# Optimization experiments

Hardware: AMD Instinct MI355X
Metric: run time of the kernel (lower is better)

## Reference

```python
import jax, jax.numpy as jnp
import numpy as np

NEG_SLOPE = 0.2
EPS = 1e-16


def gat_layer(x, src, dst, W, att_src, att_dst, bias, heads, concat):
    N = x.shape[0]
    C = W.shape[1] // heads
    h = (x @ W).reshape(N, heads, C)                      # [N,H,C]
    a_src = (h * att_src).sum(-1)                         # [N,H]
    a_dst = (h * att_dst).sum(-1)                         # [N,H]
    e = jax.nn.leaky_relu(a_src[src] + a_dst[dst], NEG_SLOPE)  # [E,H]
    # numerically-stable softmax over incoming edges of each dst node
    e_max = jax.ops.segment_max(e, dst, num_segments=N)   # [N,H]
    e_max = jnp.where(jnp.isfinite(e_max), e_max, 0.0)
    ex = jnp.exp(e - e_max[dst])                          # [E,H]
    denom = jax.ops.segment_sum(ex, dst, num_segments=N) + EPS
    alpha = ex / denom[dst]                               # [E,H]
    msg = alpha[:, :, None] * h[src]                      # [E,H,C]
    out = jax.ops.segment_sum(msg, dst, num_segments=N)   # [N,H,C]
    if concat:
        return out.reshape(N, heads * C) + bias
    return out.mean(axis=1) + bias


def setup_inputs() -> dict:
    key = jax.random.key(0)
    ks = jax.random.split(key, 12)
    N, E = 50000, 800000
    IN, HID, OUT, H = 128, 8, 40, 8
    x = jax.random.normal(ks[0], (N, IN), dtype=jnp.float32)
    edge_index = jax.random.randint(ks[1], (2, E), 0, N, dtype=jnp.int64)
    s1 = 1.0 / np.sqrt(IN)
    s2 = 1.0 / np.sqrt(HID * H)
    W1 = jax.random.normal(ks[2], (IN, H * HID), dtype=jnp.float32) * s1
    att_src1 = jax.random.normal(ks[3], (H, HID), dtype=jnp.float32) * 0.1
    att_dst1 = jax.random.normal(ks[4], (H, HID), dtype=jnp.float32) * 0.1
    bias1 = jnp.zeros((H * HID,), dtype=jnp.float32)
    W2 = jax.random.normal(ks[5], (H * HID, OUT), dtype=jnp.float32) * s2
    att_src2 = jax.random.normal(ks[6], (1, OUT), dtype=jnp.float32) * 0.1
    att_dst2 = jax.random.normal(ks[7], (1, OUT), dtype=jnp.float32) * 0.1
    bias2 = jnp.zeros((OUT,), dtype=jnp.float32)
    return {"x": x, "edge_index": edge_index,
            "W1": W1, "att_src1": att_src1, "att_dst1": att_dst1, "bias1": bias1,
            "W2": W2, "att_src2": att_src2, "att_dst2": att_dst2, "bias2": bias2}


def reference(x, edge_index, W1, att_src1, att_dst1, bias1, W2, att_src2, att_dst2, bias2):
    src, dst = edge_index[0], edge_index[1]
    # eval mode: dropout is identity
    h = gat_layer(x, src, dst, W1, att_src1, att_dst1, bias1, heads=8, concat=True)
    h = jax.nn.elu(h)
    out = gat_layer(h, src, dst, W2, att_src2, att_dst2, bias2, heads=1, concat=False)
    return out
```

## Files before the change

kernel.cpp:

```cpp
#include <hip/hip_runtime.h>
#include <math.h>

#define EPS 1e-16f
#define SLOT 64
__device__ __forceinline__ float lrelu(float v) { return v > 0.0f ? v : 0.2f * v; }

__device__ __forceinline__ unsigned short f2bf(float f) {
    unsigned u = __float_as_uint(f);
    u += 0x7FFF + ((u >> 16) & 1);
    return (unsigned short)(u >> 16);
}
__device__ __forceinline__ float bf2f(unsigned short s) {
    return __uint_as_float(((unsigned)s) << 16);
}

#define LDP 65
__global__ __launch_bounds__(256, 4) void k_gemm1_scat(
    const float* __restrict__ x, const float* __restrict__ W1,
    const float* __restrict__ att_src1, const float* __restrict__ att_dst1,
    unsigned short* __restrict__ h1b, float* __restrict__ a_src1, float* __restrict__ a_dst1,
    int N, int D, const int* __restrict__ src, const int* __restrict__ dst,
    int* __restrict__ deg, int* __restrict__ ssrc, int E) {
    __shared__ float sX[64 * LDP];
    __shared__ float sW[64 * LDP];
    int t = threadIdx.x;
    if (blockIdx.x < D) {
        int e0 = (blockIdx.x * 256 + t) * 8;
        if (e0 < E) {
            int4 sa = *((const int4*)(src + e0));
            int4 sb = *((const int4*)(src + e0 + 4));
            int4 da = *((const int4*)(dst + e0));
            int4 db = *((const int4*)(dst + e0 + 4));
            int p0 = atomicAdd(&deg[da.x], 1);
            int p1 = atomicAdd(&deg[da.y], 1);
            int p2 = atomicAdd(&deg[da.z], 1);
            int p3 = atomicAdd(&deg[da.w], 1);
            int p4 = atomicAdd(&deg[db.x], 1);
            int p5 = atomicAdd(&deg[db.y], 1);
            int p6 = atomicAdd(&deg[db.z], 1);
            int p7 = atomicAdd(&deg[db.w], 1);
            if (p0 < SLOT) ssrc[(da.x << 6) + p0] = sa.x;
            if (p1 < SLOT) ssrc[(da.y << 6) + p1] = sa.y;
            if (p2 < SLOT) ssrc[(da.z << 6) + p2] = sa.z;
            if (p3 < SLOT) ssrc[(da.w << 6) + p3] = sa.w;
            if (p4 < SLOT) ssrc[(db.x << 6) + p4] = sb.x;
            if (p5 < SLOT) ssrc[(db.y << 6) + p5] = sb.y;
            if (p6 < SLOT) ssrc[(db.z << 6) + p6] = sb.z;
            if (p7 < SLOT) ssrc[(db.w << 6) + p7] = sb.w;
        }
        return;
    }
    int r0 = (blockIdx.x - D) * 64;
    int tx = t & 15, ty = t >> 4;
    float c[4][4] = {{0.f}};
#pragma unroll
    for (int kh = 0; kh < 2; kh++) {
        for (int i = t; i < 1024; i += 256) {
            int k = i >> 4, n4 = i & 15;
            float4 v = ((const float4*)W1)[(64 * kh + k) * 16 + n4];
            float* p = sW + k * LDP + 4 * n4;
            p[0] = v.x; p[1] = v.y; p[2] = v.z; p[3] = v.w;
        }
        for (int i = t; i < 1024; i += 256) {
            int m = i >> 4, k4 = i & 15;
            int r = r0 + m;
            float4 v = make_float4(0.f, 0.f, 0.f, 0.f);
            if (r < N) v = ((const float4*)(x + (size_t)r * 128))[16 * kh + k4];
            float* p = sX + m * LDP + 4 * k4;
            p[0] = v.x; p[1] = v.y; p[2] = v.z; p[3] = v.w;
        }
        __syncthreads();
        const float* pA = sX + 4 * tx * LDP;
        const float* pB = sW + 4 * ty;
#pragma unroll 8
        for (int k = 0; k < 64; k++) {
            float a0 = pA[k], a1 = pA[LDP + k], a2 = pA[2 * LDP + k], a3 = pA[3 * LDP + k];
            const float* pb = pB + k * LDP;
            float b0 = pb[0], b1 = pb[1], b2 = pb[2], b3 = pb[3];
            c[0][0] = fmaf(a0, b0, c[0][0]); c[0][1] = fmaf(a0, b1, c[0][1]);
            c[0][2] = fmaf(a0, b2, c[0][2]); c[0][3] = fmaf(a0, b3, c[0][3]);
            c[1][0] = fmaf(a1, b0, c[1][0]); c[1][1] = fmaf(a1, b1, c[1][1]);
            c[1][2] = fmaf(a1, b2, c[1][2]); c[1][3] = fmaf(a1, b3, c[1][3]);
            c[2][0] = fmaf(a2, b0, c[2][0]); c[2][1] = fmaf(a2, b1, c[2][1]);
            c[2][2] = fmaf(a2, b2, c[2][2]); c[2][3] = fmaf(a2, b3, c[2][3]);
            c[3][0] = fmaf(a3, b0, c[3][0]); c[3][1] = fmaf(a3, b1, c[3][1]);
            c[3][2] = fmaf(a3, b2, c[3][2]); c[3][3] = fmaf(a3, b3, c[3][3]);
        }
        __syncthreads();
    }
    float as0 = att_src1[4 * ty + 0], as1 = att_src1[4 * ty + 1],
          as2 = att_src1[4 * ty + 2], as3 = att_src1[4 * ty + 3];
    float ad0 = att_dst1[4 * ty + 0], ad1 = att_dst1[4 * ty + 1],
          ad2 = att_dst1[4 * ty + 2], ad3 = att_dst1[4 * ty + 3];
    float* sPs = sX;
    float* sPd = sX + 64 * 17;
#pragma unroll
    for (int i = 0; i < 4; i++) {
        int row = 4 * tx + i;
        int r = r0 + row;
        if (r < N) {
            ushort4 hv;
            hv.x = f2bf(c[i][0]); hv.y = f2bf(c[i][1]);
            hv.z = f2bf(c[i][2]); hv.w = f2bf(c[i][3]);
            *((ushort4*)(h1b + (size_t)r * 64 + 4 * ty)) = hv;
        }
        sPs[row * 17 + ty] = fmaf(c[i][0], as0, fmaf(c[i][1], as1, fmaf(c[i][2], as2, c[i][3] * as3)));
        sPd[row * 17 + ty] = fmaf(c[i][0], ad0, fmaf(c[i][1], ad1, fmaf(c[i][2], ad2, c[i][3] * ad3)));
    }
    __syncthreads();
    for (int i = t; i < 512; i += 256) {
        int row = i >> 3, h = i & 7;
        int r = r0 + row;
        if (r < N) {
            a_src1[r * 8 + h] = sPs[row * 17 + 2 * h] + sPs[row * 17 + 2 * h + 1];
            a_dst1[r * 8 + h] = sPd[row * 17 + 2 * h] + sPd[row * 17 + 2 * h + 1];
        }
    }
}

__global__ __launch_bounds__(256) void k_node_agg1(
    const int* __restrict__ deg, const int* __restrict__ ssrc,
    const float* __restrict__ a_src1, const float* __restrict__ a_dst1,
    const unsigned short* __restrict__ h1b, const float* __restrict__ bias1,
    float* __restrict__ xx, int N) {
    int d = (blockIdx.x * 256 + threadIdx.x) >> 6;
    int lane = threadIdx.x & 63;
    if (d >= N) return;
    int start = d << 6;
    int m = min(deg[d], SLOT);
    int h8 = lane & 7;
    int eoff = lane >> 3;
    int q = lane & 31;
    int hsel = q >> 2;
    int sub = lane >> 5;
    float adst8 = a_dst1[d * 8 + h8];
    int s_lane = 0;
    if (lane < m) s_lane = ssrc[start + lane];
    int nch = (m + 7) >> 3;
    unsigned rA[4];
#pragma unroll
    for (int k = 0; k < 4; k++) {
        int sR = __shfl(s_lane, 2 * k + sub);
        rA[k] = *((const unsigned*)(h1b + (size_t)sR * 64 + (q << 1)));
    }
    float exv[8];
    float lsumA = 0.0f;
#pragma unroll
    for (int c = 0; c < 8; c++) {
        int idx = c * 8 + eoff;
        int s_c = __shfl(s_lane, idx);
        float e = 0.0f;
        if (idx < m) e = __expf(lrelu(a_src1[(size_t)s_c * 8 + h8] + adst8));
        exv[c] = e;
        lsumA += e;
    }
    float accLo = 0.0f, accHi = 0.0f;
#pragma unroll
    for (int c = 0; c < 8; c++) {
        if (c >= nch) break;
        unsigned rB[4];
        if (c + 1 < nch) {
#pragma unroll
            for (int k = 0; k < 4; k++) {
                int sR = __shfl(s_lane, (c + 1) * 8 + 2 * k + sub);
                rB[k] = *((const unsigned*)(h1b + (size_t)sR * 64 + (q << 1)));
            }
        }
#pragma unroll
        for (int k = 0; k < 4; k++) {
            float f = __shfl(exv[c], ((2 * k + sub) << 3) | hsel);
            accLo = fmaf(f, bf2f((unsigned short)(rA[k] & 0xffff)), accLo);
            accHi = fmaf(f, bf2f((unsigned short)(rA[k] >> 16)), accHi);
        }
        if (c + 1 < nch) {
#pragma unroll
            for (int k = 0; k < 4; k++) rA[k] = rB[k];
        }
    }
    accLo += __shfl_xor(accLo, 32);
    accHi += __shfl_xor(accHi, 32);
    float t = lsumA;
    t += __shfl_xor(t, 8); t += __shfl_xor(t, 16); t += __shfl_xor(t, 32);
    float lsum = __shfl(t, hsel);
    if (lane < 32) {
        float2 bz = ((const float2*)bias1)[q];
        float oLo = accLo / (lsum + EPS) + bz.x;
        float oHi = accHi / (lsum + EPS) + bz.y;
        oLo = oLo > 0.0f ? oLo : expm1f(oLo);
        oHi = oHi > 0.0f ? oHi : expm1f(oHi);
        *((float2*)(xx + (size_t)d * 64 + 2 * q)) = make_float2(oLo, oHi);
    }
}

#define LDK2 65
#define LDN2 41
__global__ __launch_bounds__(256, 2) void k_gemm2(
    const float* __restrict__ xx, const float* __restrict__ W2,
    const float* __restrict__ att_src2, const float* __restrict__ att_dst2,
    float* __restrict__ h2, float* __restrict__ a_src2, float* __restrict__ a_dst2, int N) {
    __shared__ float sX[64 * LDK2];
    __shared__ float sW[64 * LDN2];
    int t = threadIdx.x;
    int r0 = blockIdx.x * 64;
    for (int i = t; i < 640; i += 256) {
        int k = i / 10, n4 = i - k * 10;
        float4 v = ((const float4*)W2)[i];
        float* p = sW + k * LDN2 + 4 * n4;
        p[0] = v.x; p[1] = v.y; p[2] = v.z; p[3] = v.w;
    }
    for (int i = t; i < 1024; i += 256) {
        int m = i >> 4, k4 = i & 15;
        int r = r0 + m;
        float4 v = make_float4(0.f, 0.f, 0.f, 0.f);
        if (r < N) v = ((const float4*)(xx + (size_t)r * 64))[k4];
        float* p = sX + m * LDK2 + 4 * k4;
        p[0] = v.x; p[1] = v.y; p[2] = v.z; p[3] = v.w;
    }
    __syncthreads();
    int tx = t & 15, ty = t >> 4;
    bool act = ty < 10;
    float c[4][4] = {{0.f}};
    if (act) {
        const float* pA = sX + 4 * tx * LDK2;
        const float* pB = sW + 4 * ty;
#pragma unroll 8
        for (int k = 0; k < 64; k++) {
            float a0 = pA[k], a1 = pA[LDK2 + k], a2 = pA[2 * LDK2 + k], a3 = pA[3 * LDK2 + k];
            const float* pb = pB + k * LDN2;
            float b0 = pb[0], b1 = pb[1], b2 = pb[2], b3 = pb[3];
            c[0][0] = fmaf(a0, b0, c[0][0]); c[0][1] = fmaf(a0, b1, c[0][1]);
            c[0][2] = fmaf(a0, b2, c[0][2]); c[0][3] = fmaf(a0, b3, c[0][3]);
            c[1][0] = fmaf(a1, b0, c[1][0]); c[1][1] = fmaf(a1, b1, c[1][1]);
            c[1][2] = fmaf(a1, b2, c[1][2]); c[1][3] = fmaf(a1, b3, c[1][3]);
            c[2][0] = fmaf(a2, b0, c[2][0]); c[2][1] = fmaf(a2, b1, c[2][1]);
            c[2][2] = fmaf(a2, b2, c[2][2]); c[2][3] = fmaf(a2, b3, c[2][3]);
            c[3][0] = fmaf(a3, b0, c[3][0]); c[3][1] = fmaf(a3, b1, c[3][1]);
            c[3][2] = fmaf(a3, b2, c[3][2]); c[3][3] = fmaf(a3, b3, c[3][3]);
        }
    }
    float as0 = 0.f, as1 = 0.f, as2 = 0.f, as3 = 0.f;
    float ad0 = 0.f, ad1 = 0.f, ad2 = 0.f, ad3 = 0.f;
    if (act) {
        as0 = att_src2[4 * ty + 0]; as1 = att_src2[4 * ty + 1];
        as2 = att_src2[4 * ty + 2]; as3 = att_src2[4 * ty + 3];
        ad0 = att_dst2[4 * ty + 0]; ad1 = att_dst2[4 * ty + 1];
        ad2 = att_dst2[4 * ty + 2]; ad3 = att_dst2[4 * ty + 3];
    }
    __syncthreads();
    float* sPs = sX;
    float* sPd = sX + 64 * 11;
#pragma unroll
    for (int i = 0; i < 4; i++) {
        int row = 4 * tx + i;
        int r = r0 + row;
        if (act) {
            if (r < N) {
                float4 hv = make_float4(c[i][0], c[i][1], c[i][2], c[i][3]);
                *((float4*)(h2 + (size_t)r * 40 + 4 * ty)) = hv;
            }
            sPs[row * 11 + ty] = fmaf(c[i][0], as0, fmaf(c[i][1], as1, fmaf(c[i][2], as2, c[i][3] * as3)));
            sPd[row * 11 + ty] = fmaf(c[i][0], ad0, fmaf(c[i][1], ad1, fmaf(c[i][2], ad2, c[i][3] * ad3)));
        }
    }
    __syncthreads();
    if (t < 64) {
        int r = r0 + t;
        if (r < N) {
            float ps = 0.f, pd = 0.f;
#pragma unroll
            for (int j = 0; j < 10; j++) {
                ps += sPs[t * 11 + j];
                pd += sPd[t * 11 + j];
            }
            a_src2[r] = ps;
            a_dst2[r] = pd;
        }
    }
}

__global__ __launch_bounds__(256) void k_node_agg2(
    const int* __restrict__ deg, const int* __restrict__ ssrc,
    const float* __restrict__ a_src2, const float* __restrict__ a_dst2,
    const float* __restrict__ h2, const float* __restrict__ bias2,
    float* __restrict__ out, int N) {
    int d = (blockIdx.x * 256 + threadIdx.x) >> 6;
    int lane = threadIdx.x & 63;
    if (d >= N) return;
    int start = d << 6;
    int m = min(deg[d], SLOT);
    float adst = a_dst2[d];
    int s_l = 0; float ex_l = 0.0f;
    if (lane < m) {
        s_l = ssrc[start + lane];
        ex_l = __expf(lrelu(a_src2[s_l] + adst));
    }
    int grp = lane / 20;
    int q20 = lane - grp * 20;
    bool gact = grp < 3;
    int nin = (m + 2) / 3;
    int nblk = (nin + 3) >> 2;
    float aLo = 0.0f, aHi = 0.0f;
    auto loadb = [&](int b, float2* g, float* f) {
#pragma unroll
        for (int k2 = 0; k2 < 4; k2++) {
            int j = 3 * (4 * b + k2) + grp;
            int jm = j & 63;
            int sR = __shfl(s_l, jm);
            float fv = __shfl(ex_l, jm);
            f[k2] = (gact && j < m) ? fv : 0.0f;
            g[k2] = *((const float2*)(h2 + (size_t)sR * 40 + 2 * q20));
        }
    };
    float2 gA[4]; float fA[4];
    if (nblk > 0) loadb(0, gA, fA);
#pragma unroll
    for (int b = 0; b < 6; b++) {
        if (b >= nblk) break;
        float2 gB[4]; float fB[4];
        if (b + 1 < nblk) loadb(b + 1, gB, fB);
#pragma unroll
        for (int k2 = 0; k2 < 4; k2++) {
            aLo = fmaf(fA[k2], gA[k2].x, aLo);
            aHi = fmaf(fA[k2], gA[k2].y, aHi);
        }
        if (b + 1 < nblk) {
#pragma unroll
            for (int k2 = 0; k2 < 4; k2++) { gA[k2] = gB[k2]; fA[k2] = fB[k2]; }
        }
    }
    int i1 = (lane + 20) & 63, i2 = (lane + 40) & 63;
    float ml1 = __shfl(aLo, i1), ml2 = __shfl(aLo, i2);
    float mh1 = __shfl(aHi, i1), mh2 = __shfl(aHi, i2);
    aLo += ml1 + ml2;
    aHi += mh1 + mh2;
    float t = ex_l;
#pragma unroll
    for (int off = 32; off; off >>= 1) t += __shfl_xor(t, off);
    if (lane < 20) {
        float2 bz = ((const float2*)bias2)[lane];
        float oLo = aLo / (t + EPS) + bz.x;
        float oHi = aHi / (t + EPS) + bz.y;
        *((float2*)(out + (size_t)d * 40 + 2 * lane)) = make_float2(oLo, oHi);
    }
}

extern "C" void kernel_launch(void* const* d_in, const int* in_sizes, int n_in,
                              void* d_out, int out_size, void* d_ws, size_t ws_size,
                              hipStream_t stream) {
    const float* x        = (const float*)d_in[0];
    const int*   ei       = (const int*)d_in[1];
    const float* W1       = (const float*)d_in[2];
    const float* att_src1 = (const float*)d_in[3];
    const float* att_dst1 = (const float*)d_in[4];
    const float* bias1    = (const float*)d_in[5];
    const float* W2       = (const float*)d_in[6];
    const float* att_src2 = (const float*)d_in[7];
    const float* att_dst2 = (const float*)d_in[8];
    const float* bias2    = (const float*)d_in[9];
    float* out = (float*)d_out;

    const int N = in_sizes[0] / 128;
    const int E = in_sizes[1] / 2;
    const int* src = ei;
    const int* dst = ei + E;

    float* ws = (float*)d_ws;
    size_t off = 0;
    int*   deg      = (int*)(ws + off); off += (size_t)N;
    int*   ssrc     = (int*)(ws + off); off += (size_t)N * SLOT;
    unsigned short* h1b = (unsigned short*)(ws + off); off += (size_t)N * 32;
    float* a_src1   = ws + off; off += (size_t)N * 8;
    float* a_dst1   = ws + off; off += (size_t)N * 8;
    float* xx       = ws + off; off += (size_t)N * 64;
    float* h2       = ws + off; off += (size_t)N * 40;
    float* a_src2   = ws + off; off += (size_t)N;
    float* a_dst2   = ws + off; off += (size_t)N;

    const int B = 256;
    int G1 = (N + 63) / 64;
    int D  = (E / 8 + 255) / 256;

    hipMemsetAsync(deg, 0, (size_t)N * sizeof(int), stream);
    k_gemm1_scat<<<D + G1, B, 0, stream>>>(x, W1, att_src1, att_dst1, h1b, a_src1, a_dst1,
                                           N, D, src, dst, deg, ssrc, E);
    k_node_agg1<<<(N + 3) / 4, B, 0, stream>>>(deg, ssrc, a_src1, a_dst1, h1b, bias1, xx, N);
    k_gemm2<<<G1, B, 0, stream>>>(xx, W2, att_src2, att_dst2, h2, a_src2, a_dst2, N);
    k_node_agg2<<<(N + 3) / 4, B, 0, stream>>>(deg, ssrc, a_src2, a_dst2, h2, bias2, out, N);
}
```

Before: 216.3 us.

## Reassociate layer-2 GEMM after aggregation and fuse attention projections into agg1

Removes the separate layer-2 GEMM kernel by using linearity. Layer 2 now aggregates the bf16 layer-1 activations and applies W2 per destination node afterwards. The layer-2 attention scores are computed inside agg1 from precomputed W2·att vectors, which an extra block of the first kernel produces. Adjacency source indices are also stored as 16-bit and activations as bf16, cutting gather traffic. The risks are bf16 rounding of the intermediate, and source indices silently truncating if N exceeds 65535.

After: 232.5 us. 7.5% more time.

```diff
diff --git a/kernel.cpp b/kernel.cpp
--- a/kernel.cpp
+++ b/kernel.cpp
@@ -18,12 +18,27 @@
 __global__ __launch_bounds__(256, 4) void k_gemm1_scat(
     const float* __restrict__ x, const float* __restrict__ W1,
     const float* __restrict__ att_src1, const float* __restrict__ att_dst1,
+    const float* __restrict__ W2, const float* __restrict__ att_src2,
+    const float* __restrict__ att_dst2,
     unsigned short* __restrict__ h1b, float* __restrict__ a_src1, float* __restrict__ a_dst1,
-    int N, int D, const int* __restrict__ src, const int* __restrict__ dst,
-    int* __restrict__ deg, int* __restrict__ ssrc, int E) {
+    float* __restrict__ w2s, float* __restrict__ w2d,
+    int N, int D, int G1, const int* __restrict__ src, const int* __restrict__ dst,
+    int* __restrict__ deg, unsigned short* __restrict__ ssrc16, int E) {
     __shared__ float sX[64 * LDP];
     __shared__ float sW[64 * LDP];
     int t = threadIdx.x;
+    if (blockIdx.x == D + G1) {
+        if (t < 64) {
+            float s = 0.f, dd = 0.f;
+            for (int j = 0; j < 40; j++) {
+                float w = W2[t * 40 + j];
+                s = fmaf(w, att_src2[j], s);
+                dd = fmaf(w, att_dst2[j], dd);
+            }
+            w2s[t] = s; w2d[t] = dd;
+        }
+        return;
+    }
     if (blockIdx.x < D) {
         int e0 = (blockIdx.x * 256 + t) * 8;
         if (e0 < E) {
@@ -39,14 +54,14 @@
             int p5 = atomicAdd(&deg[db.y], 1);
             int p6 = atomicAdd(&deg[db.z], 1);
             int p7 = atomicAdd(&deg[db.w], 1);
-            if (p0 < SLOT) ssrc[(da.x << 6) + p0] = sa.x;
-            if (p1 < SLOT) ssrc[(da.y << 6) + p1] = sa.y;
-            if (p2 < SLOT) ssrc[(da.z << 6) + p2] = sa.z;
-            if (p3 < SLOT) ssrc[(da.w << 6) + p3] = sa.w;
-            if (p4 < SLOT) ssrc[(db.x << 6) + p4] = sb.x;
-            if (p5 < SLOT) ssrc[(db.y << 6) + p5] = sb.y;
-            if (p6 < SLOT) ssrc[(db.z << 6) + p6] = sb.z;
-            if (p7 < SLOT) ssrc[(db.w << 6) + p7] = sb.w;
+            if (p0 < SLOT) ssrc16[(da.x << 6) + p0] = (unsigned short)sa.x;
+            if (p1 < SLOT) ssrc16[(da.y << 6) + p1] = (unsigned short)sa.y;
+            if (p2 < SLOT) ssrc16[(da.z << 6) + p2] = (unsigned short)sa.z;
+            if (p3 < SLOT) ssrc16[(da.w << 6) + p3] = (unsigned short)sa.w;
+            if (p4 < SLOT) ssrc16[(db.x << 6) + p4] = (unsigned short)sb.x;
+            if (p5 < SLOT) ssrc16[(db.y << 6) + p5] = (unsigned short)sb.y;
+            if (p6 < SLOT) ssrc16[(db.z << 6) + p6] = (unsigned short)sb.z;
+            if (p7 < SLOT) ssrc16[(db.w << 6) + p7] = (unsigned short)sb.w;
         }
         return;
     }
@@ -119,10 +134,12 @@
 }
 
 __global__ __launch_bounds__(256) void k_node_agg1(
-    const int* __restrict__ deg, const int* __restrict__ ssrc,
+    const int* __restrict__ deg, const unsigned short* __restrict__ ssrc16,
     const float* __restrict__ a_src1, const float* __restrict__ a_dst1,
     const unsigned short* __restrict__ h1b, const float* __restrict__ bias1,
-    float* __restrict__ xx, int N) {
+    const float* __restrict__ w2s, const float* __restrict__ w2d,
+    unsigned short* __restrict__ xxb, float* __restrict__ a_src2, float* __restrict__ a_dst2,
+    int N) {
     int d = (blockIdx.x * 256 + threadIdx.x) >> 6;
     int lane = threadIdx.x & 63;
     if (d >= N) return;
@@ -135,7 +152,7 @@
     int sub = lane >> 5;
     float adst8 = a_dst1[d * 8 + h8];
     int s_lane = 0;
-    if (lane < m) s_lane = ssrc[start + lane];
+    if (lane < m) s_lane = ssrc16[start + lane];
     int nch = (m + 7) >> 3;
     unsigned rA[4];
 #pragma unroll
@@ -182,166 +199,91 @@
     float t = lsumA;
     t += __shfl_xor(t, 8); t += __shfl_xor(t, 16); t += __shfl_xor(t, 32);
     float lsum = __shfl(t, hsel);
+    float ps = 0.f, pd = 0.f;
     if (lane < 32) {
         float2 bz = ((const float2*)bias1)[q];
         float oLo = accLo / (lsum + EPS) + bz.x;
         float oHi = accHi / (lsum + EPS) + bz.y;
         oLo = oLo > 0.0f ? oLo : expm1f(oLo);
         oHi = oHi > 0.0f ? oHi : expm1f(oHi);
-        *((float2*)(xx + (size_t)d * 64 + 2 * q)) = make_float2(oLo, oHi);
-    }
-}
-
-#define LDK2 65
-#define LDN2 41
-__global__ __launch_bounds__(256, 2) void k_gemm2(
-    const float* __restrict__ xx, const float* __restrict__ W2,
-    const float* __restrict__ att_src2, const float* __restrict__ att_dst2,
-    float* __restrict__ h2, float* __restrict__ a_src2, float* __restrict__ a_dst2, int N) {
-    __shared__ float sX[64 * LDK2];
-    __shared__ float sW[64 * LDN2];
-    int t = threadIdx.x;
-    int r0 = blockIdx.x * 64;
-    for (int i = t; i < 640; i += 256) {
-        int k = i / 10, n4 = i - k * 10;
-        float4 v = ((const float4*)W2)[i];
-        float* p = sW + k * LDN2 + 4 * n4;
-        p[0] = v.x; p[1] = v.y; p[2] = v.z; p[3] = v.w;
-    }
-    for (int i = t; i < 1024; i += 256) {
-        int m = i >> 4, k4 = i & 15;
-        int r = r0 + m;
-        float4 v = make_float4(0.f, 0.f, 0.f, 0.f);
-        if (r < N) v = ((const float4*)(xx + (size_t)r * 64))[k4];
-        float* p = sX + m * LDK2 + 4 * k4;
-        p[0] = v.x; p[1] = v.y; p[2] = v.z; p[3] = v.w;
-    }
-    __syncthreads();
-    int tx = t & 15, ty = t >> 4;
-    bool act = ty < 10;
-    float c[4][4] = {{0.f}};
-    if (act) {
-        const float* pA = sX + 4 * tx * LDK2;
-        const float* pB = sW + 4 * ty;
-#pragma unroll 8
-        for (int k = 0; k < 64; k++) {
-            float a0 = pA[k], a1 = pA[LDK2 + k], a2 = pA[2 * LDK2 + k], a3 = pA[3 * LDK2 + k];
-            const float* pb = pB + k * LDN2;
-            float b0 = pb[0], b1 = pb[1], b2 = pb[2], b3 = pb[3];
-            c[0][0] = fmaf(a0, b0, c[0][0]); c[0][1] = fmaf(a0, b1, c[0][1]);
-            c[0][2] = fmaf(a0, b2, c[0][2]); c[0][3] = fmaf(a0, b3, c[0][3]);
-            c[1][0] = fmaf(a1, b0, c[1][0]); c[1][1] = fmaf(a1, b1, c[1][1]);
-            c[1][2] = fmaf(a1, b2, c[1][2]); c[1][3] = fmaf(a1, b3, c[1][3]);
-            c[2][0] = fmaf(a2, b0, c[2][0]); c[2][1] = fmaf(a2, b1, c[2][1]);
-            c[2][2] = fmaf(a2, b2, c[2][2]); c[2][3] = fmaf(a2, b3, c[2][3]);
-            c[3][0] = fmaf(a3, b0, c[3][0]); c[3][1] = fmaf(a3, b1, c[3][1]);
-            c[3][2] = fmaf(a3, b2, c[3][2]); c[3][3] = fmaf(a3, b3, c[3][3]);
-        }
-    }
-    float as0 = 0.f, as1 = 0.f, as2 = 0.f, as3 = 0.f;
-    float ad0 = 0.f, ad1 = 0.f, ad2 = 0.f, ad3 = 0.f;
-    if (act) {
-        as0 = att_src2[4 * ty + 0]; as1 = att_src2[4 * ty + 1];
-        as2 = att_src2[4 * ty + 2]; as3 = att_src2[4 * ty + 3];
-        ad0 = att_dst2[4 * ty + 0]; ad1 = att_dst2[4 * ty + 1];
-        ad2 = att_dst2[4 * ty + 2]; ad3 = att_dst2[4 * ty + 3];
-    }
-    __syncthreads();
-    float* sPs = sX;
-    float* sPd = sX + 64 * 11;
-#pragma unroll
-    for (int i = 0; i < 4; i++) {
-        int row = 4 * tx + i;
-        int r = r0 + row;
-        if (act) {
-            if (r < N) {
-                float4 hv = make_float4(c[i][0], c[i][1], c[i][2], c[i][3]);
-                *((float4*)(h2 + (size_t)r * 40 + 4 * ty)) = hv;
-            }
-            sPs[row * 11 + ty] = fmaf(c[i][0], as0, fmaf(c[i][1], as1, fmaf(c[i][2], as2, c[i][3] * as3)));
-            sPd[row * 11 + ty] = fmaf(c[i][0], ad0, fmaf(c[i][1], ad1, fmaf(c[i][2], ad2, c[i][3] * ad3)));
-        }
-    }
-    __syncthreads();
-    if (t < 64) {
-        int r = r0 + t;
-        if (r < N) {
-            float ps = 0.f, pd = 0.f;
-#pragma unroll
-            for (int j = 0; j < 10; j++) {
-                ps += sPs[t * 11 + j];
-                pd += sPd[t * 11 + j];
-            }
-            a_src2[r] = ps;
-            a_dst2[r] = pd;
-        }
-    }
+        unsigned pk = ((unsigned)f2bf(oHi) << 16) | (unsigned)f2bf(oLo);
+        *((unsigned*)(xxb + (size_t)d * 64 + 2 * q)) = pk;
+        float2 ws2 = ((const float2*)w2s)[q];
+        float2 wd2 = ((const float2*)w2d)[q];
+        ps = fmaf(oLo, ws2.x, oHi * ws2.y);
+        pd = fmaf(oLo, wd2.x, oHi * wd2.y);
+    }
+    ps += __shfl_xor(ps, 1); ps += __shfl_xor(ps, 2); ps += __shfl_xor(ps, 4);
+    ps += __shfl_xor(ps, 8); ps += __shfl_xor(ps, 16);
+    pd += __shfl_xor(pd, 1); pd += __shfl_xor(pd, 2); pd += __shfl_xor(pd, 4);
+    pd += __shfl_xor(pd, 8); pd += __shfl_xor(pd, 16);
+    if (lane == 0) { a_src2[d] = ps; a_dst2[d] = pd; }
 }
 
 __global__ __launch_bounds__(256) void k_node_agg2(
-    const int* __restrict__ deg, const int* __restrict__ ssrc,
+    const int* __restrict__ deg, const unsigned short* __restrict__ ssrc16,
     const float* __restrict__ a_src2, const float* __restrict__ a_dst2,
-    const float* __restrict__ h2, const float* __restrict__ bias2,
-    float* __restrict__ out, int N) {
+    const unsigned short* __restrict__ xxb, const float* __restrict__ W2,
+    const float* __restrict__ bias2, float* __restrict__ out, int N) {
     int d = (blockIdx.x * 256 + threadIdx.x) >> 6;
     int lane = threadIdx.x & 63;
     if (d >= N) return;
     int start = d << 6;
     int m = min(deg[d], SLOT);
     float adst = a_dst2[d];
-    int s_l = 0; float ex_l = 0.0f;
-    if (lane < m) {
-        s_l = ssrc[start + lane];
-        ex_l = __expf(lrelu(a_src2[s_l] + adst));
-    }
-    int grp = lane / 20;
-    int q20 = lane - grp * 20;
-    bool gact = grp < 3;
-    int nin = (m + 2) / 3;
-    int nblk = (nin + 3) >> 2;
-    float aLo = 0.0f, aHi = 0.0f;
-    auto loadb = [&](int b, float2* g, float* f) {
-#pragma unroll
-        for (int k2 = 0; k2 < 4; k2++) {
-            int j = 3 * (4 * b + k2) + grp;
-            int jm = j & 63;
-            int sR = __shfl(s_l, jm);
-            float fv = __shfl(ex_l, jm);
-            f[k2] = (gact && j < m) ? fv : 0.0f;
-            g[k2] = *((const float2*)(h2 + (size_t)sR * 40 + 2 * q20));
-        }
-    };
-    float2 gA[4]; float fA[4];
-    if (nblk > 0) loadb(0, gA, fA);
-#pragma unroll
-    for (int b = 0; b < 6; b++) {
-        if (b >= nblk) break;
-        float2 gB[4]; float fB[4];
-        if (b + 1 < nblk) loadb(b + 1, gB, fB);
-#pragma unroll
-        for (int k2 = 0; k2 < 4; k2++) {
-            aLo = fmaf(fA[k2], gA[k2].x, aLo);
-            aHi = fmaf(fA[k2], gA[k2].y, aHi);
-        }
-        if (b + 1 < nblk) {
-#pragma unroll
-            for (int k2 = 0; k2 < 4; k2++) { gA[k2] = gB[k2]; fA[k2] = fB[k2]; }
-        }
-    }
-    int i1 = (lane + 20) & 63, i2 = (lane + 40) & 63;
-    float ml1 = __shfl(aLo, i1), ml2 = __shfl(aLo, i2);
-    float mh1 = __shfl(aHi, i1), mh2 = __shfl(aHi, i2);
-    aLo += ml1 + ml2;
-    aHi += mh1 + mh2;
+    int s_lane = 0;
+    if (lane < m) s_lane = ssrc16[start + lane];
+    float ex_l = 0.0f;
+    if (lane < m) ex_l = __expf(lrelu(a_src2[s_lane] + adst));
     float t = ex_l;
 #pragma unroll
     for (int off = 32; off; off >>= 1) t += __shfl_xor(t, off);
-    if (lane < 20) {
-        float2 bz = ((const float2*)bias2)[lane];
-        float oLo = aLo / (t + EPS) + bz.x;
-        float oHi = aHi / (t + EPS) + bz.y;
-        *((float2*)(out + (size_t)d * 40 + 2 * lane)) = make_float2(oLo, oHi);
-    }
+    int q = lane & 31;
+    int sub = lane >> 5;
+    int nch = (m + 7) >> 3;
+    unsigned rA[4];
+#pragma unroll
+    for (int k = 0; k < 4; k++) {
+        int sR = __shfl(s_lane, 2 * k + sub);
+        rA[k] = *((const unsigned*)(xxb + (size_t)sR * 64 + (q << 1)));
+    }
+    float accLo = 0.0f, accHi = 0.0f;
+#pragma unroll
+    for (int c = 0; c < 8; c++) {
+        if (c >= nch) break;
+        unsigned rB[4];
+        if (c + 1 < nch) {
+#pragma unroll
+            for (int k = 0; k < 4; k++) {
+                int sR = __shfl(s_lane, (c + 1) * 8 + 2 * k + sub);
+                rB[k] = *((const unsigned*)(xxb + (size_t)sR * 64 + (q << 1)));
+            }
+        }
+#pragma unroll
+        for (int k = 0; k < 4; k++) {
+            float f = __shfl(ex_l, c * 8 + 2 * k + sub);
+            accLo = fmaf(f, bf2f((unsigned short)(rA[k] & 0xffff)), accLo);
+            accHi = fmaf(f, bf2f((unsigned short)(rA[k] >> 16)), accHi);
+        }
+        if (c + 1 < nch) {
+#pragma unroll
+            for (int k = 0; k < 4; k++) rA[k] = rB[k];
+        }
+    }
+    accLo += __shfl_xor(accLo, 32);
+    accHi += __shfl_xor(accHi, 32);
+    float yLo = accLo / (t + EPS);
+    float yHi = accHi / (t + EPS);
+    int jj = lane < 40 ? lane : 39;
+    float oj = bias2[jj];
+#pragma unroll 8
+    for (int l = 0; l < 32; l++) {
+        float yl = __shfl(yLo, l);
+        float yh = __shfl(yHi, l);
+        oj = fmaf(yl, W2[(2 * l) * 40 + jj], oj);
+        oj = fmaf(yh, W2[(2 * l + 1) * 40 + jj], oj);
+    }
+    if (lane < 40) out[(size_t)d * 40 + lane] = oj;
 }
 
 extern "C" void kernel_launch(void* const* d_in, const int* in_sizes, int n_in,
@@ -366,24 +308,27 @@
 
     float* ws = (float*)d_ws;
     size_t off = 0;
-    int*   deg      = (int*)(ws + off); off += (size_t)N;
-    int*   ssrc     = (int*)(ws + off); off += (size_t)N * SLOT;
-    unsigned short* h1b = (unsigned short*)(ws + off); off += (size_t)N * 32;
-    float* a_src1   = ws + off; off += (size_t)N * 8;
-    float* a_dst1   = ws + off; off += (size_t)N * 8;
-    float* xx       = ws + off; off += (size_t)N * 64;
-    float* h2       = ws + off; off += (size_t)N * 40;
-    float* a_src2   = ws + off; off += (size_t)N;
-    float* a_dst2   = ws + off; off += (size_t)N;
+    int*            deg    = (int*)(ws + off);            off += (size_t)N;
+    unsigned short* ssrc16 = (unsigned short*)(ws + off); off += (size_t)N * 32;
+    unsigned short* h1b    = (unsigned short*)(ws + off); off += (size_t)N * 32;
+    float* a_src1 = ws + off; off += (size_t)N * 8;
+    float* a_dst1 = ws + off; off += (size_t)N * 8;
+    unsigned short* xxb    = (unsigned short*)(ws + off); off += (size_t)N * 32;
+    float* a_src2 = ws + off; off += (size_t)N;
+    float* a_dst2 = ws + off; off += (size_t)N;
+    float* w2s    = ws + off; off += 64;
+    float* w2d    = ws + off; off += 64;
 
     const int B = 256;
     int G1 = (N + 63) / 64;
     int D  = (E / 8 + 255) / 256;
 
     hipMemsetAsync(deg, 0, (size_t)N * sizeof(int), stream);
-    k_gemm1_scat<<<D + G1, B, 0, stream>>>(x, W1, att_src1, att_dst1, h1b, a_src1, a_dst1,
-                                           N, D, src, dst, deg, ssrc, E);
-    k_node_agg1<<<(N + 3) / 4, B, 0, stream>>>(deg, ssrc, a_src1, a_dst1, h1b, bias1, xx, N);
-    k_gemm2<<<G1, B, 0, stream>>>(xx, W2, att_src2, att_dst2, h2, a_src2, a_dst2, N);
-    k_node_agg2<<<(N + 3) / 4, B, 0, stream>>>(deg, ssrc, a_src2, a_dst2, h2, bias2, out, N);
-}
+    k_gemm1_scat<<<D + G1 + 1, B, 0, stream>>>(x, W1, att_src1, att_dst1, W2, att_src2,
+                                               att_dst2, h1b, a_src1, a_dst1, w2s, w2d,
+                                               N, D, G1, src, dst, deg, ssrc16, E);
+    k_node_agg1<<<(N + 3) / 4, B, 0, stream>>>(deg, ssrc16, a_src1, a_dst1, h1b, bias1,
+                                               w2s, w2d, xxb, a_src2, a_dst2, N);
+    k_node_agg2<<<(N + 3) / 4, B, 0, stream>>>(deg, ssrc16, a_src2, a_dst2, xxb, W2,
+                                               bias2, out, N);
+}
```

## Pre-bin edges by destination modulo 8 to localize degree atomics

Applied to the files above, without the earlier changes.

Adds a binning kernel that groups edges into 8 buckets by dst&7, packing dst and src into one 32-bit word. The scatter phase then processes each bucket with a bucket-private degree array, aiming to keep atomic traffic local to one cache partition and cut contention. The cost is an extra kernel launch plus writing and re-reading the packed edge buffer. The packing assumes node ids fit in 16 bits.

Result: no change. 216.4 us (+0.0%).

```diff
diff --git a/kernel.cpp b/kernel.cpp
--- a/kernel.cpp
+++ b/kernel.cpp
@@ -12,6 +12,43 @@
 }
 __device__ __forceinline__ float bf2f(unsigned short s) {
     return __uint_as_float(((unsigned)s) << 16);
+}
+
+__global__ __launch_bounds__(256) void k_bin(
+    const int* __restrict__ src, const int* __restrict__ dst,
+    unsigned* __restrict__ bucket, int* __restrict__ cnt, int E, int CAP) {
+    __shared__ int lcnt[8];
+    __shared__ int lbase[8];
+    int t = threadIdx.x;
+    if (t < 8) lcnt[t] = 0;
+    __syncthreads();
+    int e0 = (blockIdx.x * 256 + t) * 8;
+    unsigned pk[8]; int pos[8]; int pp[8];
+    bool act = e0 < E;
+    if (act) {
+        int4 sa = *((const int4*)(src + e0));
+        int4 sb = *((const int4*)(src + e0 + 4));
+        int4 da = *((const int4*)(dst + e0));
+        int4 db = *((const int4*)(dst + e0 + 4));
+        int s[8] = {sa.x, sa.y, sa.z, sa.w, sb.x, sb.y, sb.z, sb.w};
+        int d_[8] = {da.x, da.y, da.z, da.w, db.x, db.y, db.z, db.w};
+#pragma unroll
+        for (int i = 0; i < 8; i++) {
+            pp[i] = d_[i] & 7;
+            pk[i] = ((unsigned)d_[i] << 16) | (unsigned)s[i];
+            pos[i] = atomicAdd(&lcnt[pp[i]], 1);
+        }
+    }
+    __syncthreads();
+    if (t < 8) lbase[t] = atomicAdd(&cnt[t], lcnt[t]);
+    __syncthreads();
+    if (act) {
+#pragma unroll
+        for (int i = 0; i < 8; i++) {
+            int idx = lbase[pp[i]] + pos[i];
+            if (idx < CAP) bucket[(size_t)pp[i] * CAP + idx] = pk[i];
+        }
+    }
 }
 
 #define LDP 65
@@ -19,38 +56,43 @@
     const float* __restrict__ x, const float* __restrict__ W1,
     const float* __restrict__ att_src1, const float* __restrict__ att_dst1,
     unsigned short* __restrict__ h1b, float* __restrict__ a_src1, float* __restrict__ a_dst1,
-    int N, int D, const int* __restrict__ src, const int* __restrict__ dst,
-    int* __restrict__ deg, int* __restrict__ ssrc, int E) {
+    int N, int S, const unsigned* __restrict__ bucket, const int* __restrict__ cnt,
+    int CAP, int PAL, int* __restrict__ degP, int* __restrict__ ssrc) {
     __shared__ float sX[64 * LDP];
     __shared__ float sW[64 * LDP];
     int t = threadIdx.x;
-    if (blockIdx.x < D) {
-        int e0 = (blockIdx.x * 256 + t) * 8;
-        if (e0 < E) {
-            int4 sa = *((const int4*)(src + e0));
-            int4 sb = *((const int4*)(src + e0 + 4));
-            int4 da = *((const int4*)(dst + e0));
-            int4 db = *((const int4*)(dst + e0 + 4));
-            int p0 = atomicAdd(&deg[da.x], 1);
-            int p1 = atomicAdd(&deg[da.y], 1);
-            int p2 = atomicAdd(&deg[da.z], 1);
-            int p3 = atomicAdd(&deg[da.w], 1);
-            int p4 = atomicAdd(&deg[db.x], 1);
-            int p5 = atomicAdd(&deg[db.y], 1);
-            int p6 = atomicAdd(&deg[db.z], 1);
-            int p7 = atomicAdd(&deg[db.w], 1);
-            if (p0 < SLOT) ssrc[(da.x << 6) + p0] = sa.x;
-            if (p1 < SLOT) ssrc[(da.y << 6) + p1] = sa.y;
-            if (p2 < SLOT) ssrc[(da.z << 6) + p2] = sa.z;
-            if (p3 < SLOT) ssrc[(da.w << 6) + p3] = sa.w;
-            if (p4 < SLOT) ssrc[(db.x << 6) + p4] = sb.x;
-            if (p5 < SLOT) ssrc[(db.y << 6) + p5] = sb.y;
-            if (p6 < SLOT) ssrc[(db.z << 6) + p6] = sb.z;
-            if (p7 < SLOT) ssrc[(db.w << 6) + p7] = sb.w;
+    if (blockIdx.x < S) {
+        int g = blockIdx.x & 7;
+        int j = blockIdx.x >> 3;
+        int cn = min(cnt[g], CAP);
+        int stride = (S >> 3) * 256 * 8;
+        const unsigned* bk = bucket + (size_t)g * CAP;
+        int* dg = degP + (size_t)g * PAL;
+        for (int base = (j * 256 + t) * 8; base < cn; base += stride) {
+            if (base + 8 <= cn) {
+                uint4 a = *((const uint4*)(bk + base));
+                uint4 b = *((const uint4*)(bk + base + 4));
+                unsigned e[8] = {a.x, a.y, a.z, a.w, b.x, b.y, b.z, b.w};
+                int p[8];
+#pragma unroll
+                for (int i = 0; i < 8; i++) p[i] = atomicAdd(&dg[(e[i] >> 16) >> 3], 1);
+#pragma unroll
+                for (int i = 0; i < 8; i++) {
+                    int dd = e[i] >> 16, ss = e[i] & 0xffff;
+                    if (p[i] < SLOT) ssrc[((size_t)dd << 6) + p[i]] = ss;
+                }
+            } else {
+                for (int i = base; i < cn; i++) {
+                    unsigned e = bk[i];
+                    int dd = e >> 16, ss = e & 0xffff;
+                    int p = atomicAdd(&dg[dd >> 3], 1);
+                    if (p < SLOT) ssrc[((size_t)dd << 6) + p] = ss;
+                }
+            }
         }
         return;
     }
-    int r0 = (blockIdx.x - D) * 64;
+    int r0 = (blockIdx.x - S) * 64;
     int tx = t & 15, ty = t >> 4;
     float c[4][4] = {{0.f}};
 #pragma unroll
@@ -119,7 +161,7 @@
 }
 
 __global__ __launch_bounds__(256) void k_node_agg1(
-    const int* __restrict__ deg, const int* __restrict__ ssrc,
+    const int* __restrict__ degP, int PAL, const int* __restrict__ ssrc,
     const float* __restrict__ a_src1, const float* __restrict__ a_dst1,
     const unsigned short* __restrict__ h1b, const float* __restrict__ bias1,
     float* __restrict__ xx, int N) {
@@ -127,7 +169,7 @@
     int lane = threadIdx.x & 63;
     if (d >= N) return;
     int start = d << 6;
-    int m = min(deg[d], SLOT);
+    int m = min(degP[(size_t)(d & 7) * PAL + (d >> 3)], SLOT);
     int h8 = lane & 7;
     int eoff = lane >> 3;
     int q = lane & 31;
@@ -279,7 +321,7 @@
 }
 
 __global__ __launch_bounds__(256) void k_node_agg2(
-    const int* __restrict__ deg, const int* __restrict__ ssrc,
+    const int* __restrict__ degP, int PAL, const int* __restrict__ ssrc,
     const float* __restrict__ a_src2, const float* __restrict__ a_dst2,
     const float* __restrict__ h2, const float* __restrict__ bias2,
     float* __restrict__ out, int N) {
@@ -287,7 +329,7 @@
     int lane = threadIdx.x & 63;
     if (d >= N) return;
     int start = d << 6;
-    int m = min(deg[d], SLOT);
+    int m = min(degP[(size_t)(d & 7) * PAL + (d >> 3)], SLOT);
     float adst = a_dst2[d];
     int s_l = 0; float ex_l = 0.0f;
     if (lane < m) {
@@ -364,26 +406,35 @@
     const int* src = ei;
     const int* dst = ei + E;
 
+    const int PAL = (((N + 7) / 8) + 15) & ~15;
+    const int CAP = E / 8 + 65536;
+
     float* ws = (float*)d_ws;
     size_t off = 0;
-    int*   deg      = (int*)(ws + off); off += (size_t)N;
-    int*   ssrc     = (int*)(ws + off); off += (size_t)N * SLOT;
+    int*      degP   = (int*)(ws + off);      off += (size_t)8 * PAL;
+    int*      cnt    = (int*)(ws + off);      off += 8;
+    int*      ssrc   = (int*)(ws + off);      off += (size_t)N * SLOT;
+    unsigned* bucket = (unsigned*)(ws + off); off += (size_t)8 * CAP;
     unsigned short* h1b = (unsigned short*)(ws + off); off += (size_t)N * 32;
-    float* a_src1   = ws + off; off += (size_t)N * 8;
-    float* a_dst1   = ws + off; off += (size_t)N * 8;
-    float* xx       = ws + off; off += (size_t)N * 64;
-    float* h2       = ws + off; off += (size_t)N * 40;
-    float* a_src2   = ws + off; off += (size_t)N;
-    float* a_dst2   = ws + off; off += (size_t)N;
+    float* a_src1 = ws + off; off += (size_t)N * 8;
+    float* a_dst1 = ws + off; off += (size_t)N * 8;
+    float* xx     = ws + off; off += (size_t)N * 64;
+    float* h2     = ws + off; off += (size_t)N * 40;
+    float* a_src2 = ws + off; off += (size_t)N;
+    float* a_dst2 = ws + off; off += (size_t)N;
 
     const int B = 256;
     int G1 = (N + 63) / 64;
-    int D  = (E / 8 + 255) / 256;
-
-    hipMemsetAsync(deg, 0, (size_t)N * sizeof(int), stream);
-    k_gemm1_scat<<<D + G1, B, 0, stream>>>(x, W1, att_src1, att_dst1, h1b, a_src1, a_dst1,
-                                           N, D, src, dst, deg, ssrc, E);
-    k_node_agg1<<<(N + 3) / 4, B, 0, stream>>>(deg, ssrc, a_src1, a_dst1, h1b, bias1, xx, N);
+    int NBIN = (E / 8 + 255) / 256;
+    int S = 128;
+
+    hipMemsetAsync(degP, 0, ((size_t)8 * PAL + 8) * sizeof(int), stream);
+    k_bin<<<NBIN, B, 0, stream>>>(src, dst, bucket, cnt, E, CAP);
+    k_gemm1_scat<<<S + G1, B, 0, stream>>>(x, W1, att_src1, att_dst1, h1b, a_src1, a_dst1,
+                                           N, S, bucket, cnt, CAP, PAL, degP, ssrc);
+    k_node_agg1<<<(N + 3) / 4, B, 0, stream>>>(degP, PAL, ssrc, a_src1, a_dst1, h1b, bias1,
+                                               xx, N);
     k_gemm2<<<G1, B, 0, stream>>>(xx, W2, att_src2, att_dst2, h2, a_src2, a_dst2, N);
-    k_node_agg2<<<(N + 3) / 4, B, 0, stream>>>(deg, ssrc, a_src2, a_dst2, h2, bias2, out, N);
-}
+    k_node_agg2<<<(N + 3) / 4, B, 0, stream>>>(degP, PAL, ssrc, a_src2, a_dst2, h2, bias2,
+                                               out, N);
+}
```
